# Optimization experiments

Measured on AMD Instinct MI355X. Metric: run time of the kernel, lower is better.

## Reference

```python
import jax, jax.numpy as jnp
import numpy as np

T, H, I, E, K = 2048, 1024, 4096, 8, 2
SOFTCAP = 30.0


def setup_inputs() -> dict:
    key = jax.random.key(0)
    k1, k2, k3, k4, k5 = jax.random.split(key, 5)
    scale = 0.02
    x = jax.random.normal(k1, (T, H), dtype=jnp.float32)
    gate_w = jax.random.normal(k2, (E, H), dtype=jnp.float32) * scale  # router weight [E, H]
    w1g = jax.random.normal(k3, (E, I, H), dtype=jnp.float32) * scale  # gate proj
    w1u = jax.random.normal(k4, (E, I, H), dtype=jnp.float32) * scale  # up proj
    w2 = jax.random.normal(k5, (E, H, I), dtype=jnp.float32) * scale   # down proj
    return {"x": x, "gate_w": gate_w, "w1g": w1g, "w1u": w1u, "w2": w2}


def reference(x, gate_w, w1g, w1u, w2):
    # --- Router: fp32 logits, tanh softcap, softmax, top-k (no renormalize) ---
    logits = x.astype(jnp.float32) @ gate_w.T            # [T, E]
    capped = SOFTCAP * jnp.tanh(logits / SOFTCAP)
    probs = jax.nn.softmax(capped, axis=-1)              # [T, E]
    topk_w, topk_ids = jax.lax.top_k(probs, K)           # [T, K], [T, K]
    topk_w = topk_w.astype(x.dtype)

    # --- Experts: gated GLU FFN with erf-GELU, weighted combine ---
    out = jnp.zeros_like(x)
    for e in range(E):  # E is a small structural constant
        we = jnp.sum(topk_w * (topk_ids == e), axis=-1)  # [T] combine weight (0 if not routed)
        g = jax.nn.gelu(x @ w1g[e].T, approximate=False)  # [T, I]
        h = g * (x @ w1u[e].T)                            # [T, I]
        out = out + (h @ w2[e].T) * we[:, None]           # [T, H]
    return out
```

## Files before the change

### kernel.cpp

```cpp
#include <hip/hip_runtime.h>
#include <hip/hip_bf16.h>
#include <stdint.h>

#define T_TOK 2048
#define H_DIM 1024
#define I_DIM 4096
#define E_NUM 8

#define GBM 256
#define BM 128
#define BN 64
#define BK 64
#define KS 2

typedef unsigned short u16;
typedef __bf16 bf16_t;
typedef bf16_t bf16x8 __attribute__((ext_vector_type(8)));
typedef float f32x4 __attribute__((ext_vector_type(4)));

__device__ __forceinline__ u16 f2bf(float f) {
  union { float f; unsigned u; } a; a.f = f;
  unsigned r = a.u + 0x7FFFu + ((a.u >> 16) & 1u);
  return (u16)(r >> 16);
}

__device__ __forceinline__ void gload_lds16(const void* g, void* l) {
  __builtin_amdgcn_global_load_lds(
      (const __attribute__((address_space(1))) void*)g,
      (__attribute__((address_space(3))) void*)l, 16, 0, 0);
}

__device__ __forceinline__ float gelu_fast(float g) {
  float y = g * (0.7978845608f + 0.0356774081f * g * g);
  return g / (1.0f + __expf(-2.0f * y));
}

__device__ __forceinline__ uint4 pack8(float4 f0, float4 f1) {
  union { uint4 u; u16 s[8]; } p;
  p.s[0] = f2bf(f0.x); p.s[1] = f2bf(f0.y); p.s[2] = f2bf(f0.z); p.s[3] = f2bf(f0.w);
  p.s[4] = f2bf(f1.x); p.s[5] = f2bf(f1.y); p.s[6] = f2bf(f1.z); p.s[7] = f2bf(f1.w);
  return p.u;
}

__global__ __launch_bounds__(256) void k_prep(const float* __restrict__ x,
                                              float* __restrict__ out,
                                              u16* __restrict__ xb,
                                              int* __restrict__ counts) {
  int i = blockIdx.x * 256 + threadIdx.x;
  if (i < E_NUM) counts[i] = 0;
  float4 v = reinterpret_cast<const float4*>(x)[i];
  ushort4 b;
  b.x = f2bf(v.x); b.y = f2bf(v.y); b.z = f2bf(v.z); b.w = f2bf(v.w);
  reinterpret_cast<ushort4*>(xb)[i] = b;
  reinterpret_cast<float4*>(out)[i] = make_float4(0.f, 0.f, 0.f, 0.f);
}

__global__ __launch_bounds__(256) void k_router(const float* __restrict__ x,
                                                const float* __restrict__ gw,
                                                int* __restrict__ counts,
                                                int* __restrict__ ids,
                                                float* __restrict__ wts) {
  int gtid = blockIdx.x * 256 + threadIdx.x;
  int t = gtid >> 6;
  int lane = threadIdx.x & 63;
  if (t >= T_TOK) return;
  const float* xr = x + (size_t)t * H_DIM;
  float4 xv[4];
#pragma unroll
  for (int j = 0; j < 4; ++j) xv[j] = reinterpret_cast<const float4*>(xr)[lane + 64 * j];
  float logit[E_NUM];
#pragma unroll
  for (int e = 0; e < E_NUM; ++e) {
    const float4* gr = reinterpret_cast<const float4*>(gw + (size_t)e * H_DIM);
    float s = 0.f;
#pragma unroll
    for (int j = 0; j < 4; ++j) {
      float4 g = gr[lane + 64 * j];
      s += xv[j].x * g.x + xv[j].y * g.y + xv[j].z * g.z + xv[j].w * g.w;
    }
#pragma unroll
    for (int off = 32; off; off >>= 1) s += __shfl_xor(s, off);
    logit[e] = s;
  }
  if (lane == 0) {
    float cap[E_NUM], mx = -1e30f;
#pragma unroll
    for (int e = 0; e < E_NUM; ++e) {
      cap[e] = 30.f * tanhf(logit[e] * (1.f / 30.f));
      mx = fmaxf(mx, cap[e]);
    }
    float p[E_NUM], sum = 0.f;
#pragma unroll
    for (int e = 0; e < E_NUM; ++e) { p[e] = expf(cap[e] - mx); sum += p[e]; }
    int i1 = 0; float p1 = p[0];
#pragma unroll
    for (int e = 1; e < E_NUM; ++e) if (p[e] > p1) { p1 = p[e]; i1 = e; }
    int i2 = -1; float p2 = -1.f;
#pragma unroll
    for (int e = 0; e < E_NUM; ++e) if (e != i1 && p[e] > p2) { p2 = p[e]; i2 = e; }
    float inv = 1.f / sum;
    int s1 = atomicAdd(&counts[i1], 1);
    ids[i1 * T_TOK + s1] = t; wts[i1 * T_TOK + s1] = p1 * inv;
    int s2 = atomicAdd(&counts[i2], 1);
    ids[i2 * T_TOK + s2] = t; wts[i2 * T_TOK + s2] = p2 * inv;
  }
}

__global__ void k_offs(const int* __restrict__ counts, int* __restrict__ offs) {
  if (threadIdx.x == 0) {
    int a = 0;
    for (int e = 0; e < E_NUM; ++e) { offs[e] = a; a += counts[e]; }
  }
}

__global__ __launch_bounds__(512) void k_gateup4(
    const u16* __restrict__ xb, const float* __restrict__ w1g, const float* __restrict__ w1u,
    const int* __restrict__ counts, const int* __restrict__ offs, const int* __restrict__ ids,
    u16* __restrict__ h) {
  const int e = blockIdx.z, mt = blockIdx.y, nt = blockIdx.x;
  const int cnt = counts[e];
  if (mt * GBM >= cnt) return;
  __shared__ u16 As[2 * GBM * BK];
  __shared__ u16 Bg[BN * BK];
  __shared__ u16 Bu[BN * BK];
  const int tid = threadIdx.x, lane = tid & 63, wid = tid >> 6;
  const int wr = (wid >> 1) * 64, wc = (wid & 1) * 32;
  const int lr = lane & 15, lk = lane >> 4;
  const int i0 = nt * BN;
  const int lrow = lane >> 3;
  const int lgs = (lane & 7) ^ (lrow & 7);
  const int sw = lr & 7;

  const u16* asrc[4];
#pragma unroll
  for (int i = 0; i < 4; ++i) {
    int rg = mt * GBM + wid * 32 + i * 8 + lrow;
    if (rg >= cnt) rg = cnt - 1;
    asrc[i] = xb + (size_t)ids[e * T_TOK + rg] * H_DIM + lgs * 8;
  }
  u16* aldsb = As + (wid * 32) * BK;

  const int br = tid >> 3, bc = tid & 7;
  const float* gsrc = w1g + (size_t)(e * I_DIM + i0 + br) * H_DIM + bc * 8;
  const float* usrc = w1u + (size_t)(e * I_DIM + i0 + br) * H_DIM + bc * 8;
  const int wgo = br * BK + (((bc) ^ (br & 7)) << 3);
  float4 RG0, RG1, RU0, RU1;
  auto LOADB = [&](int ko) {
    RG0 = *reinterpret_cast<const float4*>(gsrc + ko);
    RG1 = *reinterpret_cast<const float4*>(gsrc + ko + 4);
    RU0 = *reinterpret_cast<const float4*>(usrc + ko);
    RU1 = *reinterpret_cast<const float4*>(usrc + ko + 4);
  };
  auto WRITEB = [&]() {
    *reinterpret_cast<uint4*>(&Bg[wgo]) = pack8(RG0, RG1);
    *reinterpret_cast<uint4*>(&Bu[wgo]) = pack8(RU0, RU1);
  };
  auto STAGE_A = [&](int buf, int ko) {
#pragma unroll
    for (int i = 0; i < 4; ++i)
      gload_lds16(asrc[i] + ko, aldsb + buf * GBM * BK + i * 8 * BK);
  };

  f32x4 accg[4][2], accu[4][2];
#pragma unroll
  for (int mi = 0; mi < 4; ++mi)
#pragma unroll
    for (int ni = 0; ni < 2; ++ni) { accg[mi][ni] = (f32x4)0.f; accu[mi][ni] = (f32x4)0.f; }

  LOADB(0);
  STAGE_A(0, 0);
  WRITEB();
  __syncthreads();

  const int NT = H_DIM / BK;
  for (int kt = 0; kt < NT; ++kt) {
    const int cur = kt & 1;
    if (kt + 1 < NT) {
      LOADB((kt + 1) * BK);
      STAGE_A(cur ^ 1, (kt + 1) * BK);
    }
#pragma unroll
    for (int kk = 0; kk < 2; ++kk) {
      const int colg = kk * 4 + lk;
      const int gsw = (colg ^ sw) << 3;
      bf16x8 a[4], bg[2], bu[2];
#pragma unroll
      for (int mi = 0; mi < 4; ++mi)
        a[mi] = *reinterpret_cast<const bf16x8*>(&As[cur * GBM * BK + (wr + mi * 16 + lr) * BK + gsw]);
#pragma unroll
      for (int ni = 0; ni < 2; ++ni) {
        bg[ni] = *reinterpret_cast<const bf16x8*>(&Bg[(wc + ni * 16 + lr) * BK + gsw]);
        bu[ni] = *reinterpret_cast<const bf16x8*>(&Bu[(wc + ni * 16 + lr) * BK + gsw]);
      }
#pragma unroll
      for (int mi = 0; mi < 4; ++mi)
#pragma unroll
        for (int ni = 0; ni < 2; ++ni) {
          accg[mi][ni] = __builtin_amdgcn_mfma_f32_16x16x32_bf16(a[mi], bg[ni], accg[mi][ni], 0, 0, 0);
          accu[mi][ni] = __builtin_amdgcn_mfma_f32_16x16x32_bf16(a[mi], bu[ni], accu[mi][ni], 0, 0, 0);
        }
    }
    if (kt + 1 < NT) {
      __syncthreads();
      WRITEB();
      __syncthreads();
    }
  }

  const int hbase = offs[e];
#pragma unroll
  for (int mi = 0; mi < 4; ++mi)
#pragma unroll
    for (int rr = 0; rr < 4; ++rr) {
      int grow = mt * GBM + wr + mi * 16 + lk * 4 + rr;
      if (grow < cnt) {
        size_t hrow = (size_t)(hbase + grow) * I_DIM;
#pragma unroll
        for (int ni = 0; ni < 2; ++ni) {
          int col = i0 + wc + ni * 16 + lr;
          h[hrow + col] = f2bf(gelu_fast(accg[mi][ni][rr]) * accu[mi][ni][rr]);
        }
      }
    }
}

__global__ __launch_bounds__(256) void k_down9(
    const u16* __restrict__ h, const float* __restrict__ w2,
    const int* __restrict__ counts, const int* __restrict__ offs, const int* __restrict__ ids,
    const float* __restrict__ wts, float* __restrict__ out) {
  const int e = blockIdx.z, mt = blockIdx.y;
  const int nt = blockIdx.x & 15, ks = blockIdx.x >> 4;
  const int cnt = counts[e];
  if (mt * BM >= cnt) return;
  __shared__ u16 As[2 * BM * BK];
  __shared__ u16 Bs[BN * BK];
  const int tid = threadIdx.x, lane = tid & 63, wid = tid >> 6;
  const int wr = (wid >> 1) * 64, wc = (wid & 1) * 32;
  const int lr = lane & 15, lk = lane >> 4;
  const int n0 = nt * BN;
  const int hbase = offs[e];
  const int lrow = lane >> 3;
  const int lgs = (lane & 7) ^ (lrow & 7);
  const int sw = lr & 7;

  const u16* asrc[4];
#pragma unroll
  for (int i = 0; i < 4; ++i) {
    int rg = mt * BM + wid * 32 + i * 8 + lrow;
    if (rg >= cnt) rg = cnt - 1;
    asrc[i] = h + (size_t)(hbase + rg) * I_DIM + lgs * 8;
  }
  u16* aldsb = As + (wid * 32) * BK;

  const int brw = tid >> 2, bc4 = tid & 3;
  const float* bsrc = w2 + (size_t)(e * H_DIM + n0 + brw) * I_DIM + bc4 * 16;
  const int wg0 = brw * BK + (((bc4 * 2) ^ (brw & 7)) << 3);
  const int wg1 = brw * BK + (((bc4 * 2 + 1) ^ (brw & 7)) << 3);
  float4 RB0, RB1, RB2, RB3;
  auto LOADB = [&](int ko) {
    RB0 = *reinterpret_cast<const float4*>(bsrc + ko);
    RB1 = *reinterpret_cast<const float4*>(bsrc + ko + 4);
    RB2 = *reinterpret_cast<const float4*>(bsrc + ko + 8);
    RB3 = *reinterpret_cast<const float4*>(bsrc + ko + 12);
  };
  auto WRITEB = [&]() {
    *reinterpret_cast<uint4*>(&Bs[wg0]) = pack8(RB0, RB1);
    *reinterpret_cast<uint4*>(&Bs[wg1]) = pack8(RB2, RB3);
  };
  auto STAGE_A = [&](int buf, int ko) {
#pragma unroll
    for (int i = 0; i < 4; ++i)
      gload_lds16(asrc[i] + ko, aldsb + buf * BM * BK + i * 8 * BK);
  };

  f32x4 acc[4][2];
#pragma unroll
  for (int mi = 0; mi < 4; ++mi)
#pragma unroll
    for (int ni = 0; ni < 2; ++ni) acc[mi][ni] = (f32x4)0.f;

  const int KT = I_DIM / BK / KS;
  const int kbase = ks * KT * BK;
  LOADB(kbase);
  STAGE_A(0, kbase);
  WRITEB();
  __syncthreads();

  for (int kt = 0; kt < KT; ++kt) {
    const int cur = kt & 1;
    if (kt + 1 < KT) {
      LOADB(kbase + (kt + 1) * BK);
      STAGE_A(cur ^ 1, kbase + (kt + 1) * BK);
    }
#pragma unroll
    for (int kk = 0; kk < 2; ++kk) {
      const int colg = kk * 4 + lk;
      const int gsw = (colg ^ sw) << 3;
      bf16x8 a[4], b[2];
#pragma unroll
      for (int mi = 0; mi < 4; ++mi)
        a[mi] = *reinterpret_cast<const bf16x8*>(&As[cur * BM * BK + (wr + mi * 16 + lr) * BK + gsw]);
#pragma unroll
      for (int ni = 0; ni < 2; ++ni)
        b[ni] = *reinterpret_cast<const bf16x8*>(&Bs[(wc + ni * 16 + lr) * BK + gsw]);
#pragma unroll
      for (int mi = 0; mi < 4; ++mi)
#pragma unroll
        for (int ni = 0; ni < 2; ++ni)
          acc[mi][ni] = __builtin_amdgcn_mfma_f32_16x16x32_bf16(a[mi], b[ni], acc[mi][ni], 0, 0, 0);
    }
    if (kt + 1 < KT) {
      __syncthreads();
      WRITEB();
      __syncthreads();
    }
  }

#pragma unroll
  for (int mi = 0; mi < 4; ++mi)
#pragma unroll
    for (int rr = 0; rr < 4; ++rr) {
      int grow = mt * BM + wr + mi * 16 + lk * 4 + rr;
      if (grow < cnt) {
        int tok = ids[e * T_TOK + grow];
        float w = wts[e * T_TOK + grow];
#pragma unroll
        for (int ni = 0; ni < 2; ++ni) {
          int col = n0 + wc + ni * 16 + lr;
          atomicAdd(&out[(size_t)tok * H_DIM + col], w * acc[mi][ni][rr]);
        }
      }
    }
}

extern "C" void kernel_launch(void* const* d_in, const int* in_sizes, int n_in,
                              void* d_out, int out_size, void* d_ws, size_t ws_size,
                              hipStream_t stream) {
  const float* x   = (const float*)d_in[0];
  const float* gw  = (const float*)d_in[1];
  const float* w1g = (const float*)d_in[2];
  const float* w1u = (const float*)d_in[3];
  const float* w2  = (const float*)d_in[4];
  float* out = (float*)d_out;
  char* ws = (char*)d_ws;

  const size_t MB = 1u << 20;
  const size_t OFF_XB  = 0;
  const size_t OFF_H   = 4 * MB;
  const size_t OFF_IDS = OFF_H + 32 * MB;
  const size_t OFF_WTS = OFF_IDS + (64u << 10);
  const size_t OFF_CNT = OFF_WTS + (64u << 10);

  u16* xb     = (u16*)(ws + OFF_XB);
  u16* h      = (u16*)(ws + OFF_H);
  int* ids    = (int*)(ws + OFF_IDS);
  float* wts  = (float*)(ws + OFF_WTS);
  int* counts = (int*)(ws + OFF_CNT);
  int* offs   = counts + 8;

  k_prep<<<2048, 256, 0, stream>>>(x, out, xb, counts);
  k_router<<<512, 256, 0, stream>>>(x, gw, counts, ids, wts);
  k_offs<<<1, 64, 0, stream>>>(counts, offs);
  k_gateup4<<<dim3(I_DIM / BN, T_TOK / GBM, E_NUM), 512, 0, stream>>>(
      xb, w1g, w1u, counts, offs, ids, h);
  k_down9<<<dim3((H_DIM / BN) * KS, T_TOK / BM, E_NUM), 256, 0, stream>>>(
      h, w2, counts, offs, ids, wts, out);
}
```

Before: 303.0 us.

## Enlarge down-projection M tile to 256 rows with 512-thread blocks

```diff
diff --git a/kernel.cpp b/kernel.cpp
--- a/kernel.cpp
+++ b/kernel.cpp
@@ -8,7 +8,6 @@
 #define E_NUM 8
 
 #define GBM 256
-#define BM 128
 #define BN 64
 #define BK 64
 #define KS 2
@@ -36,9 +35,9 @@
 }
 
 __device__ __forceinline__ uint4 pack8(float4 f0, float4 f1) {
-  union { uint4 u; u16 s[8]; } p;
-  p.s[0] = f2bf(f0.x); p.s[1] = f2bf(f0.y); p.s[2] = f2bf(f0.z); p.s[3] = f2bf(f0.w);
-  p.s[4] = f2bf(f1.x); p.s[5] = f2bf(f1.y); p.s[6] = f2bf(f1.z); p.s[7] = f2bf(f1.w);
+  union { bf16x8 v; uint4 u; } p;
+  p.v[0] = (bf16_t)f0.x; p.v[1] = (bf16_t)f0.y; p.v[2] = (bf16_t)f0.z; p.v[3] = (bf16_t)f0.w;
+  p.v[4] = (bf16_t)f1.x; p.v[5] = (bf16_t)f1.y; p.v[6] = (bf16_t)f1.z; p.v[7] = (bf16_t)f1.w;
   return p.u;
 }
 
@@ -224,15 +223,15 @@
     }
 }
 
-__global__ __launch_bounds__(256) void k_down9(
+__global__ __launch_bounds__(512) void k_down10(
     const u16* __restrict__ h, const float* __restrict__ w2,
     const int* __restrict__ counts, const int* __restrict__ offs, const int* __restrict__ ids,
     const float* __restrict__ wts, float* __restrict__ out) {
   const int e = blockIdx.z, mt = blockIdx.y;
   const int nt = blockIdx.x & 15, ks = blockIdx.x >> 4;
   const int cnt = counts[e];
-  if (mt * BM >= cnt) return;
-  __shared__ u16 As[2 * BM * BK];
+  if (mt * GBM >= cnt) return;
+  __shared__ u16 As[2 * GBM * BK];
   __shared__ u16 Bs[BN * BK];
   const int tid = threadIdx.x, lane = tid & 63, wid = tid >> 6;
   const int wr = (wid >> 1) * 64, wc = (wid & 1) * 32;
@@ -246,31 +245,27 @@
   const u16* asrc[4];
 #pragma unroll
   for (int i = 0; i < 4; ++i) {
-    int rg = mt * BM + wid * 32 + i * 8 + lrow;
+    int rg = mt * GBM + wid * 32 + i * 8 + lrow;
     if (rg >= cnt) rg = cnt - 1;
     asrc[i] = h + (size_t)(hbase + rg) * I_DIM + lgs * 8;
   }
   u16* aldsb = As + (wid * 32) * BK;
 
-  const int brw = tid >> 2, bc4 = tid & 3;
-  const float* bsrc = w2 + (size_t)(e * H_DIM + n0 + brw) * I_DIM + bc4 * 16;
-  const int wg0 = brw * BK + (((bc4 * 2) ^ (brw & 7)) << 3);
-  const int wg1 = brw * BK + (((bc4 * 2 + 1) ^ (brw & 7)) << 3);
-  float4 RB0, RB1, RB2, RB3;
+  const int br = tid >> 3, bc = tid & 7;
+  const float* bsrc = w2 + (size_t)(e * H_DIM + n0 + br) * I_DIM + bc * 8;
+  const int wgo = br * BK + (((bc) ^ (br & 7)) << 3);
+  float4 RB0, RB1;
   auto LOADB = [&](int ko) {
     RB0 = *reinterpret_cast<const float4*>(bsrc + ko);
     RB1 = *reinterpret_cast<const float4*>(bsrc + ko + 4);
-    RB2 = *reinterpret_cast<const float4*>(bsrc + ko + 8);
-    RB3 = *reinterpret_cast<const float4*>(bsrc + ko + 12);
   };
   auto WRITEB = [&]() {
-    *reinterpret_cast<uint4*>(&Bs[wg0]) = pack8(RB0, RB1);
-    *reinterpret_cast<uint4*>(&Bs[wg1]) = pack8(RB2, RB3);
+    *reinterpret_cast<uint4*>(&Bs[wgo]) = pack8(RB0, RB1);
   };
   auto STAGE_A = [&](int buf, int ko) {
 #pragma unroll
     for (int i = 0; i < 4; ++i)
-      gload_lds16(asrc[i] + ko, aldsb + buf * BM * BK + i * 8 * BK);
+      gload_lds16(asrc[i] + ko, aldsb + buf * GBM * BK + i * 8 * BK);
   };
 
   f32x4 acc[4][2];
@@ -299,7 +294,7 @@
       bf16x8 a[4], b[2];
 #pragma unroll
       for (int mi = 0; mi < 4; ++mi)
-        a[mi] = *reinterpret_cast<const bf16x8*>(&As[cur * BM * BK + (wr + mi * 16 + lr) * BK + gsw]);
+        a[mi] = *reinterpret_cast<const bf16x8*>(&As[cur * GBM * BK + (wr + mi * 16 + lr) * BK + gsw]);
 #pragma unroll
       for (int ni = 0; ni < 2; ++ni)
         b[ni] = *reinterpret_cast<const bf16x8*>(&Bs[(wc + ni * 16 + lr) * BK + gsw]);
@@ -320,7 +315,7 @@
   for (int mi = 0; mi < 4; ++mi)
 #pragma unroll
     for (int rr = 0; rr < 4; ++rr) {
-      int grow = mt * BM + wr + mi * 16 + lk * 4 + rr;
+      int grow = mt * GBM + wr + mi * 16 + lk * 4 + rr;
       if (grow < cnt) {
         int tok = ids[e * T_TOK + grow];
         float w = wts[e * T_TOK + grow];
@@ -363,6 +358,6 @@
   k_offs<<<1, 64, 0, stream>>>(counts, offs);
   k_gateup4<<<dim3(I_DIM / BN, T_TOK / GBM, E_NUM), 512, 0, stream>>>(
       xb, w1g, w1u, counts, offs, ids, h);
-  k_down9<<<dim3((H_DIM / BN) * KS, T_TOK / BM, E_NUM), 256, 0, stream>>>(
+  k_down10<<<dim3((H_DIM / BN) * KS, T_TOK / GBM, E_NUM), 512, 0, stream>>>(
       h, w2, counts, offs, ids, wts, out);
 }
```

Result: slower. 315.6 us (+4.2%).
